# Kernel optimization log

Hardware: AMD Instinct MI355X
Metric: run time of the kernel (lower is better)

The kernel has to match this reference:

```python
import jax, jax.numpy as jnp
import numpy as np
import math

EMBED_DIM = 512
NUM_HEADS = 8
NUM_LAYERS = 6
MASK_SIZE = 32
KERNEL = 3
BATCH = 16
SEQ = MASK_SIZE * MASK_SIZE
DFF = EMBED_DIM  # dim_feedforward=embed_dim in the original
LN_EPS = 1e-5


def make_window_mask(size, kernel_size):
    # Faithful port of Transformer.generate_window_mask (additive -inf mask
    # implementing a kernel_size x kernel_size window over a size x size grid).
    pad = kernel_size // 2
    cols = [-math.inf] * pad + list(range(size)) + [-math.inf] * pad
    pad_cols = [-math.inf] * len(cols)
    rows = [pad_cols] + [[i * size + v for v in cols] for i in range(size)] + [pad_cols]
    rows = [[int(v) if v >= 0 else -1 for v in row] for row in rows]
    grid = np.array(rows, dtype=np.int64)
    mask = np.full((size * size, size * size), -np.inf, dtype=np.float32)
    r = 0
    for y in range(size):
        for x in range(size):
            idx = grid[y:y + kernel_size, x:x + kernel_size].reshape(-1)
            idx = idx[idx >= 0]
            mask[r, idx] = 0.0
            r += 1
    return jnp.asarray(mask)


def setup_inputs() -> dict:
    key = jax.random.key(0)
    ks = jax.random.split(key, 14)
    D, F, L = EMBED_DIM, DFF, NUM_LAYERS
    s = 0.02
    inp = {
        "x": jax.random.normal(ks[0], (BATCH, SEQ, D), dtype=jnp.float32),
        "ln1_g": jnp.ones((L, D), jnp.float32),
        "ln1_b": jnp.zeros((L, D), jnp.float32),
        "wqkv": jax.random.normal(ks[1], (L, 3 * D, D), jnp.float32) * s,
        "bqkv": jnp.zeros((L, 3 * D), jnp.float32),
        "wo": jax.random.normal(ks[2], (L, D, D), jnp.float32) * s,
        "bo": jnp.zeros((L, D), jnp.float32),
        "ln2_g": jnp.ones((L, D), jnp.float32),
        "ln2_b": jnp.zeros((L, D), jnp.float32),
        "w1": jax.random.normal(ks[3], (L, F, D), jnp.float32) * s,
        "b1": jnp.zeros((L, F), jnp.float32),
        "w2": jax.random.normal(ks[4], (L, D, F), jnp.float32) * s,
        "b2": jnp.zeros((L, D), jnp.float32),
        "mask": make_window_mask(MASK_SIZE, KERNEL),
    }
    return inp


def _layer_norm(x, g, b):
    m = jnp.mean(x, axis=-1, keepdims=True)
    v = jnp.mean((x - m) ** 2, axis=-1, keepdims=True)
    return (x - m) / jnp.sqrt(v + LN_EPS) * g + b


def _encoder(x, mask, ln1_g, ln1_b, wqkv, bqkv, wo, bo, ln2_g, ln2_b, w1, b1, w2, b2):
    # norm_first TransformerEncoderLayer, eval mode (dropout = no-op), gelu(exact)
    H = NUM_HEADS

    def layer(h, p):
        g1, bb1, wq, bq, wo_, bo_, g2, bb2, w1_, b1_, w2_, b2_ = p
        B, S, D = h.shape
        dh = D // H
        n = _layer_norm(h, g1, bb1)
        qkv = n @ wq.T + bq                      # [B,S,3D]
        q, k, v = jnp.split(qkv, 3, axis=-1)
        q = q.reshape(B, S, H, dh)
        k = k.reshape(B, S, H, dh)
        v = v.reshape(B, S, H, dh)
        scores = jnp.einsum("bqhd,bkhd->bhqk", q, k) / math.sqrt(dh) + mask
        attn = jax.nn.softmax(scores, axis=-1)
        o = jnp.einsum("bhqk,bkhd->bqhd", attn, v).reshape(B, S, D)
        h = h + (o @ wo_.T + bo_)
        n2 = _layer_norm(h, g2, bb2)
        ff = jax.nn.gelu(n2 @ w1_.T + b1_, approximate=False) @ w2_.T + b2_
        return h + ff, None

    out, _ = jax.lax.scan(
        layer, x, (ln1_g, ln1_b, wqkv, bqkv, wo, bo, ln2_g, ln2_b, w1, b1, w2, b2)
    )
    return out


def reference(x, ln1_g, ln1_b, wqkv, bqkv, wo, bo, ln2_g, ln2_b, w1, b1, w2, b2, mask):
    return _encoder(x, mask, ln1_g, ln1_b, wqkv, bqkv, wo, bo, ln2_g, ln2_b, w1, b1, w2, b2)
```

## Files before the change

kernel.cpp:

```cpp
#include <hip/hip_runtime.h>
#include <math.h>

#define BATCH   16
#define SEQ     1024
#define DIM     512
#define NH      8
#define DHEAD   64
#define NLAYER  6
#define MROWS   (BATCH * SEQ)
#define GR      32
#define KDIM    512
#define CHUNKB  8
#define CHUNKM  (CHUNKB * SEQ)

#define ASTRIP  4
#define KSLOTS  6
#define LSTR    68

typedef __attribute__((ext_vector_type(8))) short          bf16x8;
typedef __attribute__((ext_vector_type(4))) float          f32x4;
typedef __attribute__((ext_vector_type(8))) unsigned short u16x8;

__device__ __forceinline__ unsigned short bf16rn(float f) {
    unsigned u = __float_as_uint(f);
    u += 0x7FFFu + ((u >> 16) & 1u);
    return (unsigned short)(u >> 16);
}
__device__ __forceinline__ float bf16tof(unsigned short h) {
    return __uint_as_float(((unsigned)h) << 16);
}

__device__ __forceinline__ void gload16(const void* g, void* l) {
    __builtin_amdgcn_global_load_lds(
        (const __attribute__((address_space(1))) void*)g,
        (__attribute__((address_space(3))) void*)l,
        16, 0, 0);
}

__global__ __launch_bounds__(256)
void pack_w(const float* __restrict__ W, unsigned short* __restrict__ out,
            int NT, int nlu) {
    int gid  = blockIdx.x * 256 + threadIdx.x;
    int l    = gid / nlu;
    if (l >= NLAYER) return;
    int rem  = gid - l * nlu;
    int nt   = rem >> 14;
    int r2   = rem & 16383;
    int kt   = (r2 >> 10) & 15;
    int s    = (r2 >> 6) & 15;
    int lane = r2 & 63;
    int hl = s >> 3, f = s & 7;
    int row = nt * 128 + f * 16 + (lane & 15);
    int k   = kt * 32 + (lane >> 4) * 8;
    int N   = NT * 128;
    const float* src = W + ((size_t)l * N + row) * 512 + k;
    float4 a = ((const float4*)src)[0];
    float4 b = ((const float4*)src)[1];
    float v[8] = {a.x, a.y, a.z, a.w, b.x, b.y, b.z, b.w};
    u16x8 o;
    #pragma unroll
    for (int j = 0; j < 8; j++) {
        unsigned short hh = bf16rn(v[j]);
        o[j] = hl ? bf16rn(v[j] - bf16tof(hh)) : hh;
    }
    *(u16x8*)(out + (size_t)gid * 8) = o;
}

__global__ __launch_bounds__(256)
void ln_split(const float* __restrict__ x, const float* __restrict__ g,
              const float* __restrict__ b, unsigned short* __restrict__ oh,
              unsigned short* __restrict__ ol) {
    int w    = (blockIdx.x * 256 + threadIdx.x) >> 6;
    int lane = threadIdx.x & 63;
    const float* row = x + (size_t)w * DIM;
    float4 v0 = ((const float4*)row)[lane];
    float4 v1 = ((const float4*)row)[lane + 64];

    float s = v0.x + v0.y + v0.z + v0.w + v1.x + v1.y + v1.z + v1.w;
    #pragma unroll
    for (int o = 32; o; o >>= 1) s += __shfl_xor(s, o, 64);
    float mean = s * (1.0f / DIM);

    float d0x = v0.x - mean, d0y = v0.y - mean, d0z = v0.z - mean, d0w = v0.w - mean;
    float d1x = v1.x - mean, d1y = v1.y - mean, d1z = v1.z - mean, d1w = v1.w - mean;
    float vv = d0x*d0x + d0y*d0y + d0z*d0z + d0w*d0w
             + d1x*d1x + d1y*d1y + d1z*d1z + d1w*d1w;
    #pragma unroll
    for (int o = 32; o; o >>= 1) vv += __shfl_xor(vv, o, 64);
    float r = rsqrtf(vv * (1.0f / DIM) + 1e-5f);

    float4 g0 = ((const float4*)g)[lane];
    float4 g1 = ((const float4*)g)[lane + 64];
    float4 b0 = ((const float4*)b)[lane];
    float4 b1 = ((const float4*)b)[lane + 64];

    float o0x = d0x * r * g0.x + b0.x, o0y = d0y * r * g0.y + b0.y;
    float o0z = d0z * r * g0.z + b0.z, o0w = d0w * r * g0.w + b0.w;
    float o1x = d1x * r * g1.x + b1.x, o1y = d1y * r * g1.y + b1.y;
    float o1z = d1z * r * g1.z + b1.z, o1w = d1w * r * g1.w + b1.w;

    ushort4 h0, l0, h1, l1;
    h0.x = bf16rn(o0x); l0.x = bf16rn(o0x - bf16tof(h0.x));
    h0.y = bf16rn(o0y); l0.y = bf16rn(o0y - bf16tof(h0.y));
    h0.z = bf16rn(o0z); l0.z = bf16rn(o0z - bf16tof(h0.z));
    h0.w = bf16rn(o0w); l0.w = bf16rn(o0w - bf16tof(h0.w));
    h1.x = bf16rn(o1x); l1.x = bf16rn(o1x - bf16tof(h1.x));
    h1.y = bf16rn(o1y); l1.y = bf16rn(o1y - bf16tof(h1.y));
    h1.z = bf16rn(o1z); l1.z = bf16rn(o1z - bf16tof(h1.z));
    h1.w = bf16rn(o1w); l1.w = bf16rn(o1w - bf16tof(h1.w));

    ushort4* ohr = (ushort4*)(oh + (size_t)w * DIM);
    ushort4* olr = (ushort4*)(ol + (size_t)w * DIM);
    ohr[lane]      = h0;  ohr[lane + 64] = h1;
    olr[lane]      = l0;  olr[lane + 64] = l1;
}

template <int EPI>
__global__ __launch_bounds__(256, 2)
void gemm_mfma(const unsigned short* __restrict__ Ah, const unsigned short* __restrict__ Al,
               const unsigned short* __restrict__ Wpk,
               const float* __restrict__ bias,
               float* __restrict__ C,
               unsigned short* __restrict__ Oh, unsigned short* __restrict__ Ol,
               int N) {
    __shared__ __align__(16) char smem[65536];

    const int tid  = threadIdx.x;
    const int lane = tid & 63;
    const int wid  = tid >> 6;
    const int bm = blockIdx.y, bn = blockIdx.x;
    const int wm = wid >> 1, wn = wid & 1;

    const unsigned short* aptr0[4];
    #pragma unroll
    for (int i = 0; i < 4; i++) {
        int s  = i * 4 + wid;
        int hl = s >> 3, f = s & 7;
        const unsigned short* ab = hl ? Al : Ah;
        aptr0[i] = ab + (size_t)(bm * 128 + f * 16 + (lane & 15)) * KDIM + ((lane >> 4) * 8);
    }
    const unsigned short* bbase = Wpk + (size_t)bn * 131072 + lane * 8;

    f32x4 acc[4][4];
    #pragma unroll
    for (int mi = 0; mi < 4; mi++)
        #pragma unroll
        for (int ni = 0; ni < 4; ni++)
            acc[mi][ni] = (f32x4){0.f, 0.f, 0.f, 0.f};

    auto stage = [&](int kt, int buf) {
        char* sb = smem + buf * 32768;
        #pragma unroll
        for (int i = 0; i < 4; i++) {
            int s = i * 4 + wid;
            gload16(aptr0[i] + kt * 32, sb + s * 1024);
            gload16(bbase + ((kt * 16 + s) << 9), sb + 16384 + s * 1024);
        }
    };
    auto compute = [&](int buf) {
        const char* sb = smem + buf * 32768;
        bf16x8 afr[2][4], bfr[2][4];
        #pragma unroll
        for (int hl = 0; hl < 2; hl++) {
            #pragma unroll
            for (int mi = 0; mi < 4; mi++)
                afr[hl][mi] = *(const bf16x8*)(sb + (hl * 8 + wm * 4 + mi) * 1024 + lane * 16);
            #pragma unroll
            for (int ni = 0; ni < 4; ni++)
                bfr[hl][ni] = *(const bf16x8*)(sb + 16384 + (hl * 8 + wn * 4 + ni) * 1024 + lane * 16);
        }
        #pragma unroll
        for (int mi = 0; mi < 4; mi++)
            #pragma unroll
            for (int ni = 0; ni < 4; ni++) {
                acc[mi][ni] = __builtin_amdgcn_mfma_f32_16x16x32_bf16(afr[0][mi], bfr[0][ni], acc[mi][ni], 0, 0, 0);
                acc[mi][ni] = __builtin_amdgcn_mfma_f32_16x16x32_bf16(afr[0][mi], bfr[1][ni], acc[mi][ni], 0, 0, 0);
                acc[mi][ni] = __builtin_amdgcn_mfma_f32_16x16x32_bf16(afr[1][mi], bfr[0][ni], acc[mi][ni], 0, 0, 0);
            }
    };

    stage(0, 0);
    __syncthreads();

    int cur = 0;
    for (int kt = 0; kt < 15; ++kt) {
        stage(kt + 1, cur ^ 1);
        compute(cur);
        __syncthreads();
        cur ^= 1;
    }
    compute(cur);

    const int lc = lane & 15, lr = (lane >> 4) * 4;
    const int row0 = bm * 128 + wm * 64, col0 = bn * 128 + wn * 64;
    #pragma unroll
    for (int ni = 0; ni < 4; ni++) {
        int col = col0 + ni * 16 + lc;
        float bv = bias[col];
        #pragma unroll
        for (int mi = 0; mi < 4; mi++) {
            #pragma unroll
            for (int r = 0; r < 4; r++) {
                int row = row0 + mi * 16 + lr + r;
                float v = acc[mi][ni][r] + bv;
                if (EPI == 0) {
                    C[(size_t)row * N + col] = v;
                } else if (EPI == 1) {
                    C[(size_t)row * N + col] += v;
                } else {
                    float gg = 0.5f * v * (1.0f + erff(v * 0.70710678118654752440f));
                    unsigned short hh = bf16rn(gg);
                    Oh[(size_t)row * N + col] = hh;
                    Ol[(size_t)row * N + col] = bf16rn(gg - bf16tof(hh));
                }
            }
        }
    }
}

__global__ __launch_bounds__(512)
void attn_scores(const float* __restrict__ qkv, float* __restrict__ pbuf) {
    __shared__ float tile[KSLOTS * 32 * LSTR];

    const int bidx  = blockIdx.x;
    const int strip = bidx & 7;
    const int h     = (bidx >> 3) & 7;
    const int bl    = bidx >> 6;
    const int tid   = threadIdx.x;
    const int lane  = tid & 63;
    const int w     = tid >> 6;
    const int yl    = w >> 1;
    const int xh    = w & 1;
    const int dq    = lane >> 4;
    const int xl    = lane & 15;
    const int x     = xh * 16 + xl;
    const int y0    = strip * ASTRIP;

    const float* base  = qkv + (size_t)bl * SEQ * 1536;
    const float* kbase = base + 512 + h * DHEAD;

    #pragma unroll
    for (int it = 0; it < 6; it++) {
        int fi   = tid + it * 512;
        int slot = fi >> 9;
        int rem  = fi & 511;
        int nx   = rem >> 4;
        int f4   = rem & 15;
        int gy   = y0 - 1 + slot;
        float4 v = make_float4(0.f, 0.f, 0.f, 0.f);
        if (gy >= 0 && gy < GR)
            v = *(const float4*)(kbase + (size_t)(gy * GR + nx) * 1536 + f4 * 4);
        *(float4*)&tile[(slot * 32 + nx) * LSTR + f4 * 4] = v;
    }

    const int q = (y0 + yl) * GR + x;
    const float* qp = base + (size_t)q * 1536 + h * DHEAD + dq * 16;
    float4 qv[4];
    #pragma unroll
    for (int f = 0; f < 4; f++) qv[f] = ((const float4*)qp)[f];

    __syncthreads();

    float sc[9];
    #pragma unroll
    for (int i = 0; i < 9; i++) {
        const int dy = i / 3 - 1, dx = i % 3 - 1;
        const int ny = y0 + yl + dy, nx = x + dx;
        const bool vm = (ny >= 0 && ny < GR && nx >= 0 && nx < GR);
        const int nxc = min(max(nx, 0), GR - 1);
        const float* kr = &tile[((yl + dy + 1) * 32 + nxc) * LSTR + dq * 16];
        float s = 0.f;
        #pragma unroll
        for (int f = 0; f < 4; f++) {
            float4 kv = ((const float4*)kr)[f];
            s = fmaf(qv[f].x, kv.x, s);
            s = fmaf(qv[f].y, kv.y, s);
            s = fmaf(qv[f].z, kv.z, s);
            s = fmaf(qv[f].w, kv.w, s);
        }
        s += __shfl_xor(s, 16, 64);
        s += __shfl_xor(s, 32, 64);
        sc[i] = vm ? s * 0.125f : -INFINITY;
    }

    float pmax = sc[0];
    #pragma unroll
    for (int i = 1; i < 9; i++) pmax = fmaxf(pmax, sc[i]);
    float p[9], den = 0.f;
    #pragma unroll
    for (int i = 0; i < 9; i++) {
        p[i] = expf(sc[i] - pmax);
        den += p[i];
    }
    const float inv = 1.f / den;

    if (dq == 0) {
        float* pq = pbuf + ((size_t)(bl * NH + h) * 9) * SEQ + q;
        #pragma unroll
        for (int i = 0; i < 9; i++) pq[i * SEQ] = p[i] * inv;
    }
}

__global__ __launch_bounds__(256)
void attn_pv(const float* __restrict__ qkv, const float* __restrict__ pbuf,
             unsigned short* __restrict__ oh, unsigned short* __restrict__ ol,
             int b_base) {
    const int tid  = threadIdx.x;
    const int gq   = blockIdx.x * 4 + (tid >> 6);
    const int dblk = tid & 63;
    const int bl   = gq >> 10, q = gq & (SEQ - 1);
    const int y    = q >> 5,  x = q & 31;
    const int h    = dblk >> 3;

    const float* vbase = qkv + (size_t)bl * SEQ * 1536 + 1024 + dblk * 8;
    const float* pq    = pbuf + ((size_t)(bl * NH + h) * 9) * SEQ + q;

    float acc[8];
    #pragma unroll
    for (int j = 0; j < 8; j++) acc[j] = 0.f;

    #pragma unroll
    for (int i = 0; i < 9; i++) {
        const int dy  = i / 3 - 1, dx = i % 3 - 1;
        const int nyc = min(max(y + dy, 0), GR - 1);
        const int nxc = min(max(x + dx, 0), GR - 1);
        const float w = pq[i * SEQ];
        const float* vr = vbase + (size_t)(nyc * GR + nxc) * 1536;
        float4 a = *(const float4*)(vr);
        float4 b = *(const float4*)(vr + 4);
        acc[0] = fmaf(w, a.x, acc[0]); acc[1] = fmaf(w, a.y, acc[1]);
        acc[2] = fmaf(w, a.z, acc[2]); acc[3] = fmaf(w, a.w, acc[3]);
        acc[4] = fmaf(w, b.x, acc[4]); acc[5] = fmaf(w, b.y, acc[5]);
        acc[6] = fmaf(w, b.z, acc[6]); acc[7] = fmaf(w, b.w, acc[7]);
    }

    const size_t orow = ((size_t)(b_base + bl) * SEQ + q) * DIM + dblk * 8;
    u16x8 hv, lv;
    #pragma unroll
    for (int j = 0; j < 8; j++) {
        float v = acc[j];
        unsigned short hh = bf16rn(v);
        hv[j] = hh;
        lv[j] = bf16rn(v - bf16tof(hh));
    }
    *(u16x8*)(oh + orow) = hv;
    *(u16x8*)(ol + orow) = lv;
}

extern "C" void kernel_launch(void* const* d_in, const int* in_sizes, int n_in,
                              void* d_out, int out_size, void* d_ws, size_t ws_size,
                              hipStream_t stream) {
    const float* x     = (const float*)d_in[0];
    const float* ln1_g = (const float*)d_in[1];
    const float* ln1_b = (const float*)d_in[2];
    const float* wqkv  = (const float*)d_in[3];
    const float* bqkv  = (const float*)d_in[4];
    const float* wo    = (const float*)d_in[5];
    const float* bo    = (const float*)d_in[6];
    const float* ln2_g = (const float*)d_in[7];
    const float* ln2_b = (const float*)d_in[8];
    const float* w1    = (const float*)d_in[9];
    const float* b1    = (const float*)d_in[10];
    const float* w2    = (const float*)d_in[11];
    const float* b2    = (const float*)d_in[12];

    char* ws = (char*)d_ws;
    unsigned short* wqkv_pk = (unsigned short*)ws;
    unsigned short* wo_pk   = (unsigned short*)(ws + 18874368);
    unsigned short* w1_pk   = (unsigned short*)(ws + 25165824);
    unsigned short* w2_pk   = (unsigned short*)(ws + 31457280);
    unsigned short* Ah      = (unsigned short*)(ws + 37748736);
    unsigned short* Al      = Ah + 8388608;
    float*          qkvb    = (float*)(ws + 71303168);
    unsigned short* Fh      = (unsigned short*)(ws + 71303168);
    unsigned short* Fl      = Fh + 8388608;
    float*          pbuf    = (float*)(ws + 121634816);

    float* h = (float*)d_out;

    hipMemcpyAsync(h, x, sizeof(float) * (size_t)MROWS * DIM,
                   hipMemcpyDeviceToDevice, stream);

    pack_w<<<4608, 256, 0, stream>>>(wqkv, wqkv_pk, 12, 12 * 16384);
    pack_w<<<1536, 256, 0, stream>>>(wo,   wo_pk,   4,  4 * 16384);
    pack_w<<<1536, 256, 0, stream>>>(w1,   w1_pk,   4,  4 * 16384);
    pack_w<<<1536, 256, 0, stream>>>(w2,   w2_pk,   4,  4 * 16384);

    const int LN_BLOCKS = MROWS / 4;
    const int SC_BLOCKS = CHUNKB * NH * (GR / ASTRIP);
    const int PV_BLOCKS = CHUNKM / 4;

    for (int l = 0; l < NLAYER; l++) {
        const unsigned short* Wqp = wqkv_pk + (size_t)l * 12 * 131072;
        const unsigned short* Wop = wo_pk   + (size_t)l * 4 * 131072;
        const unsigned short* W1p = w1_pk   + (size_t)l * 4 * 131072;
        const unsigned short* W2p = w2_pk   + (size_t)l * 4 * 131072;

        ln_split<<<LN_BLOCKS, 256, 0, stream>>>(h, ln1_g + l * DIM, ln1_b + l * DIM, Ah, Al);

        for (int c = 0; c < 2; c++) {
            gemm_mfma<0><<<dim3(12, 64), 256, 0, stream>>>(
                Ah + (size_t)c * CHUNKM * DIM, Al + (size_t)c * CHUNKM * DIM,
                Wqp, bqkv + l * 1536, qkvb, nullptr, nullptr, 1536);
            attn_scores<<<SC_BLOCKS, 512, 0, stream>>>(qkvb, pbuf);
            attn_pv<<<PV_BLOCKS, 256, 0, stream>>>(qkvb, pbuf, Ah, Al, c * CHUNKB);
        }

        gemm_mfma<1><<<dim3(4, 128), 256, 0, stream>>>(
            Ah, Al, Wop, bo + l * DIM, h, nullptr, nullptr, 512);

        ln_split<<<LN_BLOCKS, 256, 0, stream>>>(h, ln2_g + l * DIM, ln2_b + l * DIM, Ah, Al);

        gemm_mfma<2><<<dim3(4, 128), 256, 0, stream>>>(
            Ah, Al, W1p, b1 + l * DIM, nullptr, Fh, Fl, 512);

        gemm_mfma<1><<<dim3(4, 128), 256, 0, stream>>>(
            Fh, Fl, W2p, b2 + l * DIM, h, nullptr, nullptr, 512);
    }
}
```

Measured before the change: 1.893 ms.

## Stage GEMM epilogue through LDS for coalesced stores and remap blocks per XCD

The GEMM epilogue now writes accumulators into a swizzled LDS tile, then stores to global memory with wide, row-contiguous float4 or 8-wide bf16 writes. This replaces the scattered per-element stores and read-modify-writes of the MFMA fragment layout. The grid also becomes 1-D, and block indices are remapped so that consecutive tiles land on the same XCD (blockIdx & 7 interleave), which is meant to improve L2 reuse of A and W. The cost is an extra LDS round trip and barrier per block, and the remap assumes the grid size divides by 8.

Result: faster. 1.710 ms (-9.7%).

```diff
diff --git a/kernel.cpp b/kernel.cpp
--- a/kernel.cpp
+++ b/kernel.cpp
@@ -35,6 +35,10 @@
         (const __attribute__((address_space(1))) void*)g,
         (__attribute__((address_space(3))) void*)l,
         16, 0, 0);
+}
+
+__device__ __forceinline__ float gelu_exact(float v) {
+    return 0.5f * v * (1.0f + erff(v * 0.70710678118654752440f));
 }
 
 __global__ __launch_bounds__(256)
@@ -128,7 +132,11 @@
     const int tid  = threadIdx.x;
     const int lane = tid & 63;
     const int wid  = tid >> 6;
-    const int bm = blockIdx.y, bn = blockIdx.x;
+
+    const int ntb = N >> 7;
+    const int t   = (blockIdx.x & 7) * ((int)gridDim.x >> 3) + (blockIdx.x >> 3);
+    const int bm  = t / ntb, bn = t - bm * ntb;
+
     const int wm = wid >> 1, wn = wid & 1;
 
     const unsigned short* aptr0[4];
@@ -191,29 +199,61 @@
     }
     compute(cur);
 
-    const int lc = lane & 15, lr = (lane >> 4) * 4;
-    const int row0 = bm * 128 + wm * 64, col0 = bn * 128 + wn * 64;
-    #pragma unroll
-    for (int ni = 0; ni < 4; ni++) {
-        int col = col0 + ni * 16 + lc;
-        float bv = bias[col];
-        #pragma unroll
-        for (int mi = 0; mi < 4; mi++) {
+    __syncthreads();
+    float* ct = (float*)smem;
+    {
+        const int lc = lane & 15, lr4 = (lane >> 4) << 2;
+        #pragma unroll
+        for (int ni = 0; ni < 4; ni++) {
+            int col_l = wn * 64 + ni * 16 + lc;
+            float bv = bias[bn * 128 + col_l];
             #pragma unroll
-            for (int r = 0; r < 4; r++) {
-                int row = row0 + mi * 16 + lr + r;
-                float v = acc[mi][ni][r] + bv;
-                if (EPI == 0) {
-                    C[(size_t)row * N + col] = v;
-                } else if (EPI == 1) {
-                    C[(size_t)row * N + col] += v;
-                } else {
-                    float gg = 0.5f * v * (1.0f + erff(v * 0.70710678118654752440f));
-                    unsigned short hh = bf16rn(gg);
-                    Oh[(size_t)row * N + col] = hh;
-                    Ol[(size_t)row * N + col] = bf16rn(gg - bf16tof(hh));
+            for (int mi = 0; mi < 4; mi++) {
+                #pragma unroll
+                for (int r = 0; r < 4; r++) {
+                    int row_l = wm * 64 + mi * 16 + lr4 + r;
+                    int sc = col_l ^ (((row_l >> 2) & 1) << 4);
+                    ct[row_l * 128 + sc] = acc[mi][ni][r] + bv;
                 }
             }
+        }
+    }
+    __syncthreads();
+
+    if (EPI == 2) {
+        #pragma unroll
+        for (int i = 0; i < 8; i++) {
+            int rl  = i * 16 + (tid >> 4);
+            int c8  = (tid & 15) * 8;
+            int swz = ((rl >> 2) & 1) << 4;
+            float4 a = *(float4*)&ct[rl * 128 + (c8 ^ swz)];
+            float4 b = *(float4*)&ct[rl * 128 + ((c8 + 4) ^ swz)];
+            float vv[8] = {a.x, a.y, a.z, a.w, b.x, b.y, b.z, b.w};
+            u16x8 hv, lv;
+            #pragma unroll
+            for (int j = 0; j < 8; j++) {
+                float g = gelu_exact(vv[j]);
+                unsigned short hh = bf16rn(g);
+                hv[j] = hh;
+                lv[j] = bf16rn(g - bf16tof(hh));
+            }
+            size_t off = (size_t)(bm * 128 + rl) * N + bn * 128 + c8;
+            *(u16x8*)(Oh + off) = hv;
+            *(u16x8*)(Ol + off) = lv;
+        }
+    } else {
+        #pragma unroll
+        for (int i = 0; i < 16; i++) {
+            int rl  = i * 8 + (tid >> 5);
+            int c4  = (tid & 31) * 4;
+            int swz = ((rl >> 2) & 1) << 4;
+            float4 v = *(float4*)&ct[rl * 128 + (c4 ^ swz)];
+            float* cp = C + (size_t)(bm * 128 + rl) * N + bn * 128 + c4;
+            if (EPI == 1) {
+                float4 o = *(float4*)cp;
+                v.x += o.x; v.y += o.y; v.z += o.z; v.w += o.w;
+            }
+            *(float4*)cp = v;
         }
     }
 }
@@ -399,22 +439,22 @@
         ln_split<<<LN_BLOCKS, 256, 0, stream>>>(h, ln1_g + l * DIM, ln1_b + l * DIM, Ah, Al);
 
         for (int c = 0; c < 2; c++) {
-            gemm_mfma<0><<<dim3(12, 64), 256, 0, stream>>>(
+            gemm_mfma<0><<<768, 256, 0, stream>>>(
                 Ah + (size_t)c * CHUNKM * DIM, Al + (size_t)c * CHUNKM * DIM,
                 Wqp, bqkv + l * 1536, qkvb, nullptr, nullptr, 1536);
             attn_scores<<<SC_BLOCKS, 512, 0, stream>>>(qkvb, pbuf);
             attn_pv<<<PV_BLOCKS, 256, 0, stream>>>(qkvb, pbuf, Ah, Al, c * CHUNKB);
         }
 
-        gemm_mfma<1><<<dim3(4, 128), 256, 0, stream>>>(
+        gemm_mfma<1><<<512, 256, 0, stream>>>(
             Ah, Al, Wop, bo + l * DIM, h, nullptr, nullptr, 512);
 
         ln_split<<<LN_BLOCKS, 256, 0, stream>>>(h, ln2_g + l * DIM, ln2_b + l * DIM, Ah, Al);
 
-        gemm_mfma<2><<<dim3(4, 128), 256, 0, stream>>>(
+        gemm_mfma<2><<<512, 256, 0, stream>>>(
             Ah, Al, W1p, b1 + l * DIM, nullptr, Fh, Fl, 512);
 
-        gemm_mfma<1><<<dim3(4, 128), 256, 0, stream>>>(
+        gemm_mfma<1><<<512, 256, 0, stream>>>(
             Fh, Fl, W2p, b2 + l * DIM, h, nullptr, nullptr, 512);
     }
 }
```
